# Kernel tuning notes

Measured on AMD Instinct MI355X. Metric: run time of the kernel, lower is better.

Reference implementation:

```python
import jax, jax.numpy as jnp
import numpy as np

N_NODES = 2048
N_EDGES = 8192
EDGE_DIM = 10
EDGE_HIDDEN = 32
HID = 160


def nnconv(x, edge_index, edge_attr, w1, b1, w2, b2, root, bias):
    """PyG-style NNConv with aggr='mean'.
    x: [N, HID], edge_attr: [E, EDGE_DIM], edge_index: [2, E] (src, dst).
    Per-edge weight W_e = MLP(e) reshaped to [HID, HID]; message = x[src] @ W_e,
    mean-aggregated at dst, plus root transform and bias.
    """
    n = x.shape[0]
    h = jax.nn.relu(edge_attr @ w1 + b1)                     # [E, EDGE_HIDDEN]
    W = (h @ w2 + b2).reshape(-1, HID, HID)                  # [E, HID, HID]
    src, dst = edge_index[0], edge_index[1]
    msg = jnp.einsum('ei,eio->eo', x[src], W)                # [E, HID]
    summed = jax.ops.segment_sum(msg, dst, num_segments=n)   # [N, HID]
    cnt = jax.ops.segment_sum(jnp.ones((msg.shape[0],), x.dtype), dst,
                              num_segments=n)
    aggr = summed / jnp.maximum(cnt, 1.0)[:, None]           # mean; 0 for isolated
    return aggr + x @ root + bias


def setup_inputs() -> dict:
    key = jax.random.key(0)
    ks = jax.random.split(key, 16)
    s = 1.0 / np.sqrt(HID)
    se = 1.0 / np.sqrt(EDGE_DIM)
    sh = 1.0 / np.sqrt(EDGE_HIDDEN)
    inp = {
        'x': jax.random.normal(ks[0], (N_NODES, HID), jnp.float32),
        'edge_attr': jax.random.uniform(ks[1], (N_EDGES, EDGE_DIM), jnp.float32),
        # conv1 (subgraph_conv1) params
        'w1_a': jax.random.normal(ks[2], (EDGE_DIM, EDGE_HIDDEN), jnp.float32) * se,
        'b1_a': jnp.zeros((EDGE_HIDDEN,), jnp.float32),
        'w2_a': jax.random.normal(ks[3], (EDGE_HIDDEN, HID * HID), jnp.float32) * sh,
        'b2_a': jnp.zeros((HID * HID,), jnp.float32),
        'root_a': jax.random.normal(ks[4], (HID, HID), jnp.float32) * s,
        'bias_a': jnp.zeros((HID,), jnp.float32),
        # conv2 (subgraph_conv2, applied twice) params
        'w1_b': jax.random.normal(ks[5], (EDGE_DIM, EDGE_HIDDEN), jnp.float32) * se,
        'b1_b': jnp.zeros((EDGE_HIDDEN,), jnp.float32),
        'w2_b': jax.random.normal(ks[6], (EDGE_HIDDEN, HID * HID), jnp.float32) * sh,
        'b2_b': jnp.zeros((HID * HID,), jnp.float32),
        'root_b': jax.random.normal(ks[7], (HID, HID), jnp.float32) * s,
        'bias_b': jnp.zeros((HID,), jnp.float32),
        'edge_index': jax.random.randint(ks[8], (2, N_EDGES), 0, N_NODES, jnp.int64),
    }
    return inp


def reference(x, edge_attr, w1_a, b1_a, w2_a, b2_a, root_a, bias_a,
              w1_b, b1_b, w2_b, b2_b, root_b, bias_b, edge_index):
    # subgraph_conv1 -> ReLU -> subgraph_conv2 -> ReLU -> subgraph_conv2
    h = jax.nn.relu(nnconv(x, edge_index, edge_attr,
                           w1_a, b1_a, w2_a, b2_a, root_a, bias_a))
    h = jax.nn.relu(nnconv(h, edge_index, edge_attr,
                           w1_b, b1_b, w2_b, b2_b, root_b, bias_b))
    h = nnconv(h, edge_index, edge_attr,
               w1_b, b1_b, w2_b, b2_b, root_b, bias_b)
    return h
```

## Files before the change

kernel.cpp:

```cpp
#include <hip/hip_runtime.h>

#define NN 2048
#define NE 8192
#define ED 10
#define EH 32
#define HID 160
#define KT 5440
#define KS 10

typedef __attribute__((ext_vector_type(8))) short short8;
typedef __attribute__((ext_vector_type(4))) float f32x4;
typedef unsigned int u32;

__device__ __forceinline__ ushort f2bf(float v) {
    u32 u = __float_as_uint(v);
    u += 0x7FFF + ((u >> 16) & 1);
    return (ushort)(u >> 16);
}
__device__ __forceinline__ float bf2f(ushort u) {
    return __uint_as_float(((u32)u) << 16);
}
__device__ __forceinline__ void gl2lds16(const ushort* g, ushort* l) {
    __builtin_amdgcn_global_load_lds(
        (const __attribute__((address_space(1))) u32*)g,
        (__attribute__((address_space(3))) u32*)l, 16, 0, 0);
}

__global__ __launch_bounds__(256) void k_prep(
        const float* __restrict__ x, ushort* __restrict__ xb,
        const float* __restrict__ ea,
        const float* __restrict__ w1a, const float* __restrict__ b1a,
        const float* __restrict__ w1b, const float* __restrict__ b1b,
        float* __restrict__ ha, float* __restrict__ hb,
        const float* __restrict__ w2a, const float* __restrict__ b2a,
        const float* __restrict__ roota,
        const float* __restrict__ w2b, const float* __restrict__ b2b,
        const float* __restrict__ rootb,
        ushort* __restrict__ WcA, ushort* __restrict__ WcB,
        const int* __restrict__ ei, int* __restrict__ doff,
        int* __restrict__ degg, float* __restrict__ dinv,
        int* __restrict__ delist) {
    __shared__ char smem[20608];
    int b = blockIdx.x, t = threadIdx.x;

    if (b < 512) {
        int set = b >> 8, rel = b & 255;
        const float* w1 = set ? w1b : w1a;
        const float* b1 = set ? b1b : b1a;
        float* h = set ? hb : ha;
        int idx = rel * 1024 + t * 4;
        int e = idx >> 5, j0 = idx & 31;
        float o4[4];
#pragma unroll
        for (int u = 0; u < 4; ++u) {
            float acc = b1[j0 + u];
#pragma unroll
            for (int i = 0; i < ED; ++i) acc += ea[e * ED + i] * w1[i * EH + j0 + u];
            o4[u] = fmaxf(acc, 0.f);
        }
        *(float4*)&h[idx] = *(const float4*)o4;
        return;
    }
    if (b < 552) {
        int rel = b - 512;
        int set = rel / 20, i0 = (rel % 20) * 8;
        const float* w2 = set ? w2b : w2a;
        const float* b2 = set ? b2b : b2a;
        const float* root = set ? rootb : roota;
        ushort* W = set ? WcB : WcA;
        if (t < HID) {
#pragma unroll
            for (int di = 0; di < 8; ++di) {
                int i = i0 + di;
                u32 wv[17];
#pragma unroll
                for (int p = 0; p < 16; ++p) {
                    float v0 = w2[(size_t)(2 * p) * 25600 + i * HID + t];
                    float v1 = w2[(size_t)(2 * p + 1) * 25600 + i * HID + t];
                    wv[p] = ((u32)f2bf(v1) << 16) | f2bf(v0);
                }
                wv[16] = ((u32)f2bf(root[i * HID + t]) << 16) | f2bf(b2[i * HID + t]);
#pragma unroll
                for (int p = 0; p < 17; ++p)
                    *(u32*)&W[(size_t)t * KT + i * 34 + 2 * p] = wv[p];
            }
        }
        return;
    }
    if (b < 872) {
        int idx = (b - 552) * 1024 + t * 4;
        float4 xv = *(const float4*)&x[idx];
        ushort o4[4] = {f2bf(xv.x), f2bf(xv.y), f2bf(xv.z), f2bf(xv.w)};
        *(u32*)&xb[idx] = *(const u32*)&o4[0];
        *(u32*)&xb[idx + 2] = *(const u32*)&o4[2];
        return;
    }
    int* deg = (int*)smem;
    int* cur = deg + NN;
    int* part = cur + NN;
    for (int i = t; i < NN; i += 256) deg[i] = 0;
    __syncthreads();
    for (int e = t; e < NE; e += 256) atomicAdd(&deg[ei[NE + e]], 1);
    __syncthreads();
    int loc[8], s = 0;
#pragma unroll
    for (int i = 0; i < 8; ++i) { loc[i] = s; s += deg[t * 8 + i]; }
    part[t] = s;
    __syncthreads();
    int tot = s;
    for (int st = 1; st < 256; st <<= 1) {
        int v = (t >= st) ? part[t - st] : 0;
        __syncthreads();
        part[t] += v;
        __syncthreads();
    }
    int base = part[t] - tot;
#pragma unroll
    for (int i = 0; i < 8; ++i) {
        int d = t * 8 + i;
        doff[d] = base + loc[i];
        cur[d] = base + loc[i];
        degg[d] = deg[d];
        dinv[d] = 1.0f / fmaxf((float)deg[d], 1.0f);
    }
    __syncthreads();
    for (int e = t; e < NE; e += 256) {
        int d = ei[NE + e];
        int p = atomicAdd(&cur[d], 1);
        delist[p] = e;
    }
}

__global__ __launch_bounds__(160) void k_scatter(
        const ushort* __restrict__ xb, const float* __restrict__ h,
        const int* __restrict__ ei, const int* __restrict__ doff,
        const int* __restrict__ degg, const float* __restrict__ dinv,
        const int* __restrict__ delist, ushort* __restrict__ T) {
    __shared__ float hbuf[32 * EH];
    __shared__ int ebuf[32], sbuf[32];
    int d = blockIdx.x, t = threadIdx.x;
    int o0 = doff[d], dg = degg[d];
    float acc[33];
#pragma unroll
    for (int q = 0; q < 33; ++q) acc[q] = 0.f;
    for (int c0 = 0; c0 < dg; c0 += 32) {
        int nc = min(32, dg - c0);
        __syncthreads();
        if (t < 32 && c0 + t < dg) {
            int e = delist[o0 + c0 + t];
            ebuf[t] = e;
            sbuf[t] = ei[e];
        }
        __syncthreads();
        for (int i = t; i < nc * EH; i += 160)
            hbuf[i] = h[(size_t)ebuf[i >> 5] * EH + (i & 31)];
        __syncthreads();
        for (int j = 0; j < nc; ++j) {
            float xs = bf2f(xb[(size_t)sbuf[j] * HID + t]);
            const float* hj = &hbuf[j * EH];
#pragma unroll
            for (int q = 0; q < 32; ++q) acc[q] += hj[q] * xs;
            acc[32] += xs;
        }
    }
    float di = dinv[d];
    ushort* Trow = T + (size_t)d * KT + t * 34;
    u32 w[17];
#pragma unroll
    for (int p = 0; p < 16; ++p)
        w[p] = ((u32)f2bf(acc[2 * p + 1] * di) << 16) | f2bf(acc[2 * p] * di);
    w[16] = ((u32)xb[(size_t)d * HID + t] << 16) | f2bf(acc[32] * di);
#pragma unroll
    for (int p = 0; p < 17; ++p) *(u32*)&Trow[p * 2] = w[p];
}

__global__ __launch_bounds__(256) void k_out(const ushort* __restrict__ A,
                                             const ushort* __restrict__ B,
                                             float* __restrict__ Cp) {
    __shared__ ushort sA[128 * 32], sB[160 * 32];
    int tid = threadIdx.x;
    int bm = blockIdx.x * 128;
    int ks = blockIdx.y;
    int k0base = ks * (KT / KS);
    int wid = tid >> 6, lane = tid & 63;
    int wm = (wid >> 1) * 64, wn = (wid & 1) * 80;
    int lr = lane & 15, lk = lane >> 4;
    f32x4 acc[4][5];
#pragma unroll
    for (int i = 0; i < 4; ++i)
#pragma unroll
        for (int j = 0; j < 5; ++j) acc[i][j] = (f32x4){0.f, 0.f, 0.f, 0.f};

    for (int c = 0; c < 17; ++c) {
        int k0 = k0base + c * 32;
#pragma unroll
        for (int i = 0; i < 2; ++i) {
            int s = tid + i * 256;
            int r = s >> 2, go = (s & 3) * 8;
            gl2lds16(&A[(size_t)(bm + r) * KT + k0 + go], &sA[s * 8]);
        }
#pragma unroll
        for (int i = 0; i < 2; ++i) {
            int s = tid + i * 256;
            int r = s >> 2, go = (s & 3) * 8;
            gl2lds16(&B[(size_t)r * KT + k0 + go], &sB[s * 8]);
        }
        if (tid < 128) {
            int s = tid + 512;
            int r = s >> 2, go = (s & 3) * 8;
            gl2lds16(&B[(size_t)r * KT + k0 + go], &sB[s * 8]);
        }
        __syncthreads();
        short8 av[4], bv[5];
#pragma unroll
        for (int mt = 0; mt < 4; ++mt)
            av[mt] = *(const short8*)&sA[(wm + mt * 16 + lr) * 32 + lk * 8];
#pragma unroll
        for (int nt = 0; nt < 5; ++nt)
            bv[nt] = *(const short8*)&sB[(wn + nt * 16 + lr) * 32 + lk * 8];
#pragma unroll
        for (int mt = 0; mt < 4; ++mt)
#pragma unroll
            for (int nt = 0; nt < 5; ++nt)
                acc[mt][nt] = __builtin_amdgcn_mfma_f32_16x16x32_bf16(av[mt], bv[nt], acc[mt][nt], 0, 0, 0);
        __syncthreads();
    }
    float* Cb = Cp + (size_t)ks * NN * HID;
#pragma unroll
    for (int mt = 0; mt < 4; ++mt)
#pragma unroll
        for (int nt = 0; nt < 5; ++nt) {
            int m0 = bm + wm + mt * 16 + lk * 4;
            int n = wn + nt * 16 + lr;
#pragma unroll
            for (int r = 0; r < 4; ++r)
                Cb[(size_t)(m0 + r) * HID + n] = acc[mt][nt][r];
        }
}

__global__ __launch_bounds__(160) void k_fin(const float* __restrict__ Cp,
        const float* __restrict__ bias, ushort* __restrict__ xn,
        float* __restrict__ out, int last) {
    int d = blockIdx.x, t = threadIdx.x;
    float s = bias[t];
#pragma unroll
    for (int p = 0; p < KS; ++p) s += Cp[(size_t)p * NN * HID + d * HID + t];
    if (last) out[d * HID + t] = s;
    else      xn[d * HID + t] = f2bf(fmaxf(s, 0.f));
}

extern "C" void kernel_launch(void* const* d_in, const int* in_sizes, int n_in,
                              void* d_out, int out_size, void* d_ws, size_t ws_size,
                              hipStream_t stream) {
    const float* x     = (const float*)d_in[0];
    const float* ea    = (const float*)d_in[1];
    const float* w1a   = (const float*)d_in[2];
    const float* b1a   = (const float*)d_in[3];
    const float* w2a   = (const float*)d_in[4];
    const float* b2a   = (const float*)d_in[5];
    const float* roota = (const float*)d_in[6];
    const float* biasa = (const float*)d_in[7];
    const float* w1b   = (const float*)d_in[8];
    const float* b1b   = (const float*)d_in[9];
    const float* w2b   = (const float*)d_in[10];
    const float* b2b   = (const float*)d_in[11];
    const float* rootb = (const float*)d_in[12];
    const float* biasb = (const float*)d_in[13];
    const int*   ei    = (const int*)d_in[14];
    float* out = (float*)d_out;

    char* p = (char*)d_ws;
    ushort* T   = (ushort*)p;  p += (size_t)NN * KT * 2;
    ushort* WcA = (ushort*)p;  p += (size_t)HID * KT * 2;
    ushort* WcB = (ushort*)p;  p += (size_t)HID * KT * 2;
    float* Cp   = (float*)p;   p += (size_t)KS * NN * HID * 4;
    float* h_a  = (float*)p;   p += (size_t)NE * EH * 4;
    float* h_b  = (float*)p;   p += (size_t)NE * EH * 4;
    ushort* xb0 = (ushort*)p;  p += (size_t)NN * HID * 2;
    ushort* xn  = (ushort*)p;  p += (size_t)NN * HID * 2;
    int* doff   = (int*)p;     p += NN * 4;
    int* degg   = (int*)p;     p += NN * 4;
    float* dinv = (float*)p;   p += NN * 4;
    int* delist = (int*)p;     p += NE * 4;

    k_prep<<<873, 256, 0, stream>>>(x, xb0, ea, w1a, b1a, w1b, b1b, h_a, h_b,
                                    w2a, b2a, roota, w2b, b2b, rootb, WcA, WcB,
                                    ei, doff, degg, dinv, delist);

    struct Layer { const ushort *xin, *wc; const float *h, *bias; int last; };
    Layer L[3] = {
        {xb0, WcA, h_a, biasa, 0},
        {xn,  WcB, h_b, biasb, 0},
        {xn,  WcB, h_b, biasb, 1},
    };
    for (int l = 0; l < 3; ++l) {
        k_scatter<<<NN, 160, 0, stream>>>(L[l].xin, L[l].h, ei, doff, degg,
                                          dinv, delist, T);
        k_out<<<dim3(NN / 128, KS), 256, 0, stream>>>(T, L[l].wc, Cp);
        k_fin<<<NN, 160, 0, stream>>>(Cp, L[l].bias, xn, out, L[l].last);
    }
}
```

Measured before the change: 214.2 us.

## Double-buffer k_out LDS tiles and coalesce T/Wc row stores via shared memory

The GEMM kernel now keeps two LDS buffers and issues the global-to-LDS loads for the next K step before computing on the current one, so load latency can overlap with MFMA work. The scatter kernel and the weight-prep blocks first stage their strided 34-element-per-thread rows in shared memory, then write them out contiguously for coalesced global stores. Weight prep is spread over more blocks (2 rows each instead of 8). The cost is doubled LDS use in k_out, which may reduce occupancy, and an extra barrier plus shared-memory round trip in the scatter kernel.

Measured after the change: 201.1 us. 1.06x faster.

```diff
diff --git a/kernel.cpp b/kernel.cpp
--- a/kernel.cpp
+++ b/kernel.cpp
@@ -7,6 +7,7 @@
 #define HID 160
 #define KT 5440
 #define KS 10
+#define KSTEPS 17
 
 typedef __attribute__((ext_vector_type(8))) short short8;
 typedef __attribute__((ext_vector_type(4))) float f32x4;
@@ -40,7 +41,7 @@
         const int* __restrict__ ei, int* __restrict__ doff,
         int* __restrict__ degg, float* __restrict__ dinv,
         int* __restrict__ delist) {
-    __shared__ char smem[20608];
+    __shared__ __align__(16) char smem[21760];
     int b = blockIdx.x, t = threadIdx.x;
 
     if (b < 512) {
@@ -61,34 +62,38 @@
         *(float4*)&h[idx] = *(const float4*)o4;
         return;
     }
-    if (b < 552) {
+    if (b < 672) {
         int rel = b - 512;
-        int set = rel / 20, i0 = (rel % 20) * 8;
+        int set = rel / 80, i0 = (rel % 80) * 2;
+        u32 (*tile)[34] = (u32(*)[34])smem;
         const float* w2 = set ? w2b : w2a;
         const float* b2 = set ? b2b : b2a;
         const float* root = set ? rootb : roota;
         ushort* W = set ? WcB : WcA;
         if (t < HID) {
 #pragma unroll
-            for (int di = 0; di < 8; ++di) {
+            for (int di = 0; di < 2; ++di) {
                 int i = i0 + di;
-                u32 wv[17];
 #pragma unroll
                 for (int p = 0; p < 16; ++p) {
                     float v0 = w2[(size_t)(2 * p) * 25600 + i * HID + t];
                     float v1 = w2[(size_t)(2 * p + 1) * 25600 + i * HID + t];
-                    wv[p] = ((u32)f2bf(v1) << 16) | f2bf(v0);
+                    tile[t][di * 17 + p] = ((u32)f2bf(v1) << 16) | f2bf(v0);
                 }
-                wv[16] = ((u32)f2bf(root[i * HID + t]) << 16) | f2bf(b2[i * HID + t]);
-#pragma unroll
-                for (int p = 0; p < 17; ++p)
-                    *(u32*)&W[(size_t)t * KT + i * 34 + 2 * p] = wv[p];
+                tile[t][di * 17 + 16] = ((u32)f2bf(root[i * HID + t]) << 16) |
+                                        f2bf(b2[i * HID + t]);
             }
         }
+        __syncthreads();
+        u32* dst = (u32*)W;
+        for (int w = t; w < 5440; w += 256) {
+            int o = w / 34, j = w - o * 34;
+            dst[(size_t)o * 2720 + i0 * 17 + j] = tile[o][j];
+        }
         return;
     }
-    if (b < 872) {
-        int idx = (b - 552) * 1024 + t * 4;
+    if (b < 992) {
+        int idx = (b - 672) * 1024 + t * 4;
         float4 xv = *(const float4*)&x[idx];
         ushort o4[4] = {f2bf(xv.x), f2bf(xv.y), f2bf(xv.z), f2bf(xv.w)};
         *(u32*)&xb[idx] = *(const u32*)&o4[0];
@@ -138,6 +143,7 @@
         const int* __restrict__ delist, ushort* __restrict__ T) {
     __shared__ float hbuf[32 * EH];
     __shared__ int ebuf[32], sbuf[32];
+    __shared__ u32 rowbuf[KT / 2];
     int d = blockIdx.x, t = threadIdx.x;
     int o0 = doff[d], dg = degg[d];
     float acc[33];
@@ -146,7 +152,7 @@
     for (int c0 = 0; c0 < dg; c0 += 32) {
         int nc = min(32, dg - c0);
         __syncthreads();
-        if (t < 32 && c0 + t < dg) {
+        if (t < nc) {
             int e = delist[o0 + c0 + t];
             ebuf[t] = e;
             sbuf[t] = ei[e];
@@ -164,23 +170,22 @@
         }
     }
     float di = dinv[d];
-    ushort* Trow = T + (size_t)d * KT + t * 34;
-    u32 w[17];
 #pragma unroll
     for (int p = 0; p < 16; ++p)
-        w[p] = ((u32)f2bf(acc[2 * p + 1] * di) << 16) | f2bf(acc[2 * p] * di);
-    w[16] = ((u32)xb[(size_t)d * HID + t] << 16) | f2bf(acc[32] * di);
-#pragma unroll
-    for (int p = 0; p < 17; ++p) *(u32*)&Trow[p * 2] = w[p];
+        rowbuf[t * 17 + p] = ((u32)f2bf(acc[2 * p + 1] * di) << 16) |
+                             f2bf(acc[2 * p] * di);
+    rowbuf[t * 17 + 16] = ((u32)xb[(size_t)d * HID + t] << 16) | f2bf(acc[32] * di);
+    __syncthreads();
+    u32* Trow = (u32*)(T + (size_t)d * KT);
+    for (int w = t; w < KT / 2; w += 160) Trow[w] = rowbuf[w];
 }
 
 __global__ __launch_bounds__(256) void k_out(const ushort* __restrict__ A,
                                              const ushort* __restrict__ B,
                                              float* __restrict__ Cp) {
-    __shared__ ushort sA[128 * 32], sB[160 * 32];
+    __shared__ ushort sA[2][128 * 32], sB[2][160 * 32];
     int tid = threadIdx.x;
-    int bm = blockIdx.x * 128;
-    int ks = blockIdx.y;
+    int bm = blockIdx.x * 128, ks = blockIdx.y;
     int k0base = ks * (KT / KS);
     int wid = tid >> 6, lane = tid & 63;
     int wm = (wid >> 1) * 64, wn = (wid & 1) * 80;
@@ -191,38 +196,44 @@
 #pragma unroll
         for (int j = 0; j < 5; ++j) acc[i][j] = (f32x4){0.f, 0.f, 0.f, 0.f};
 
-    for (int c = 0; c < 17; ++c) {
+    auto stage = [&](int buf, int c) {
         int k0 = k0base + c * 32;
 #pragma unroll
         for (int i = 0; i < 2; ++i) {
             int s = tid + i * 256;
             int r = s >> 2, go = (s & 3) * 8;
-            gl2lds16(&A[(size_t)(bm + r) * KT + k0 + go], &sA[s * 8]);
+            gl2lds16(&A[(size_t)(bm + r) * KT + k0 + go], &sA[buf][s * 8]);
         }
 #pragma unroll
         for (int i = 0; i < 2; ++i) {
             int s = tid + i * 256;
             int r = s >> 2, go = (s & 3) * 8;
-            gl2lds16(&B[(size_t)r * KT + k0 + go], &sB[s * 8]);
+            gl2lds16(&B[(size_t)r * KT + k0 + go], &sB[buf][s * 8]);
         }
         if (tid < 128) {
             int s = tid + 512;
             int r = s >> 2, go = (s & 3) * 8;
-            gl2lds16(&B[(size_t)r * KT + k0 + go], &sB[s * 8]);
-        }
-        __syncthreads();
+            gl2lds16(&B[(size_t)r * KT + k0 + go], &sB[buf][s * 8]);
+        }
+    };
+    stage(0, 0);
+    __syncthreads();
+    for (int c = 0; c < KSTEPS; ++c) {
+        int cur = c & 1;
+        if (c + 1 < KSTEPS) stage(cur ^ 1, c + 1);
         short8 av[4], bv[5];
 #pragma unroll
         for (int mt = 0; mt < 4; ++mt)
-            av[mt] = *(const short8*)&sA[(wm + mt * 16 + lr) * 32 + lk * 8];
+            av[mt] = *(const short8*)&sA[cur][(wm + mt * 16 + lr) * 32 + lk * 8];
 #pragma unroll
         for (int nt = 0; nt < 5; ++nt)
-            bv[nt] = *(const short8*)&sB[(wn + nt * 16 + lr) * 32 + lk * 8];
+            bv[nt] = *(const short8*)&sB[cur][(wn + nt * 16 + lr) * 32 + lk * 8];
 #pragma unroll
         for (int mt = 0; mt < 4; ++mt)
 #pragma unroll
             for (int nt = 0; nt < 5; ++nt)
-                acc[mt][nt] = __builtin_amdgcn_mfma_f32_16x16x32_bf16(av[mt], bv[nt], acc[mt][nt], 0, 0, 0);
+                acc[mt][nt] = __builtin_amdgcn_mfma_f32_16x16x32_bf16(
+                    av[mt], bv[nt], acc[mt][nt], 0, 0, 0);
         __syncthreads();
     }
     float* Cb = Cp + (size_t)ks * NN * HID;
@@ -283,7 +294,7 @@
     float* dinv = (float*)p;   p += NN * 4;
     int* delist = (int*)p;     p += NE * 4;
 
-    k_prep<<<873, 256, 0, stream>>>(x, xb0, ea, w1a, b1a, w1b, b1b, h_a, h_b,
+    k_prep<<<993, 256, 0, stream>>>(x, xb0, ea, w1a, b1a, w1b, b1b, h_a, h_b,
                                     w2a, b2a, roota, w2b, b2b, rootb, WcA, WcB,
                                     ei, doff, degg, dinv, delist);
 
```
